# Kernel optimization log

Measured on AMD Instinct MI355X. Metric: run time of the kernel, lower is better.

## Reference

```python
import jax, jax.numpy as jnp
import numpy as np

IN_FEATURES = 16384
OUT_FEATURES = 16384
NNZ = 1_000_000
BATCH = 256


def setup_inputs() -> dict:
    key = jax.random.key(0)
    k1, k2, k3 = jax.random.split(key, 3)
    x = jax.random.normal(k1, (IN_FEATURES, BATCH), dtype=jnp.float32)
    values = jax.random.normal(k2, (NNZ,), dtype=jnp.float32)
    indices = jax.random.randint(k3, (2, NNZ), 0, OUT_FEATURES, dtype=jnp.int64)
    bias = jnp.zeros((OUT_FEATURES, 1), dtype=jnp.float32)
    return {"x": x, "values": values, "indices": indices, "bias": bias}


def reference(x, values, indices, bias):
    # Sparse (COO) matmul: out[r, :] += values[k] * x[c, :] for each nnz (r, c).
    # Equivalent to torch.sparse.mm(W_coo.coalesce(), x) + bias since
    # coalesce() sums duplicate entries and segment_sum does the same.
    row = indices[0]  # [nnz] in [0, OUT_FEATURES)
    col = indices[1]  # [nnz] in [0, IN_FEATURES)
    gathered = values[:, None] * x[col]  # [nnz, B]
    out = jax.ops.segment_sum(gathered, row, num_segments=OUT_FEATURES)  # [out, B]
    return out + bias
```

## Files before the change

### kernel.cpp

```cpp
#include <hip/hip_runtime.h>

typedef unsigned int u32;
typedef unsigned short u16;

constexpr int OUT_F = 16384;
constexpr int IN_F  = 16384;
constexpr int B_N   = 256;
constexpr int NGRP  = 256;
constexpr int GCAP  = 4608;
constexpr int BINB  = 4096;


__global__ __launch_bounds__(1024) void prep_k(
    const int* __restrict__ rows, const int* __restrict__ cols,
    const float* __restrict__ vals, const float* __restrict__ x,
    u16* __restrict__ xb, int* __restrict__ gcnt,
    uint2* __restrict__ gbuck, int nnz, int nbin, int n4) {
  const int tid = threadIdx.x;

  if ((int)blockIdx.x >= nbin) {
    const int i2 = blockIdx.x - nbin;
    for (int j = 0; j < 4; ++j) {
      int k4 = i2 * 4096 + j * 1024 + tid;
      if (k4 < n4) {
        float4 v = ((const float4*)x)[k4];
        u32 u0 = __float_as_uint(v.x), u1 = __float_as_uint(v.y),
            u2 = __float_as_uint(v.z), u3 = __float_as_uint(v.w);
        ushort4 r;
        r.x = (u16)((u0 + 0x7FFFu + ((u0 >> 16) & 1u)) >> 16);
        r.y = (u16)((u1 + 0x7FFFu + ((u1 >> 16) & 1u)) >> 16);
        r.z = (u16)((u2 + 0x7FFFu + ((u2 >> 16) & 1u)) >> 16);
        r.w = (u16)((u3 + 0x7FFFu + ((u3 >> 16) & 1u)) >> 16);
        ((ushort4*)xb)[k4] = r;
      }
    }
    return;
  }

  __shared__ int   hist[NGRP], lofs[NGRP], cur[NGRP], gbase[NGRP], scanb[NGRP];
  __shared__ uint2 stage[BINB];
  __shared__ int   tgt[BINB];

  const int base = blockIdx.x * BINB;
  const int nval = min(BINB, nnz - base);
  if (tid < NGRP) hist[tid] = 0;
  __syncthreads();

  int r[4]; u32 c[4]; float v[4]; bool ok[4];
#pragma unroll
  for (int i = 0; i < 4; ++i) {
    int k = base + i * 1024 + tid;
    ok[i] = k < nnz;
    if (ok[i]) {
      r[i] = rows[k]; c[i] = (u32)cols[k]; v[i] = vals[k];
      atomicAdd(&hist[r[i] >> 6], 1);
    }
  }
  __syncthreads();

  if (tid < NGRP) scanb[tid] = hist[tid];
  __syncthreads();
  for (int off = 1; off < NGRP; off <<= 1) {
    int t = 0;
    if (tid < NGRP && tid >= off) t = scanb[tid - off];
    __syncthreads();
    if (tid < NGRP) scanb[tid] += t;
    __syncthreads();
  }
  if (tid < NGRP) {
    int lo = scanb[tid] - hist[tid];
    lofs[tid] = lo;
    cur[tid]  = lo;
    gbase[tid] = atomicAdd(&gcnt[tid], hist[tid]);
  }
  __syncthreads();

#pragma unroll
  for (int i = 0; i < 4; ++i) {
    if (ok[i]) {
      int g   = r[i] >> 6;
      int pos = atomicAdd(&cur[g], 1);
      stage[pos].x = (c[i] << 6) | (u32)(r[i] & 63);
      stage[pos].y = __float_as_uint(v[i]);
      int w = gbase[g] + (pos - lofs[g]);
      tgt[pos] = (w < GCAP) ? (g * GCAP + w) : -1;
    }
  }
  __syncthreads();

#pragma unroll
  for (int j = 0; j < 4; ++j) {
    int idx = j * 1024 + tid;
    if (idx < nval) {
      int t = tgt[idx];
      if (t >= 0) gbuck[t] = stage[idx];
    }
  }
}

__global__ __launch_bounds__(1024) void regroup_k(
    int* __restrict__ gcnt, uint2* __restrict__ gbuck,
    int* __restrict__ rowstart, int* __restrict__ rowcnt) {
  __shared__ int hist[64], rofs[64], cur[64];
  const int tid = threadIdx.x;
  const int g   = blockIdx.x;
  int cnt = gcnt[g];
  if (cnt > GCAP) cnt = GCAP;
  uint2* bk = gbuck + (size_t)g * GCAP;

  if (tid < 64) hist[tid] = 0;
  __syncthreads();

  uint2 e[5]; bool ok[5];
#pragma unroll
  for (int i = 0; i < 5; ++i) {
    int k = i * 1024 + tid;
    ok[i] = k < cnt;
    if (ok[i]) {
      e[i] = bk[k];
      atomicAdd(&hist[e[i].x & 63u], 1);
    }
  }
  __syncthreads();

  if (tid == 0) {
    int run = 0;
    for (int b = 0; b < 64; ++b) { rofs[b] = run; cur[b] = run; run += hist[b]; }
  }
  __syncthreads();

  if (tid < 64) {
    rowstart[g * 64 + tid] = g * GCAP + rofs[tid];
    rowcnt[g * 64 + tid]   = hist[tid];
  }

#pragma unroll
  for (int i = 0; i < 5; ++i) {
    if (ok[i]) {
      int fr  = (int)(e[i].x & 63u);
      int pos = atomicAdd(&cur[fr], 1);
      bk[pos] = e[i];
    }
  }
}

__global__ __launch_bounds__(256) void spmm_final_k(
    const int* __restrict__ rowstart, const int* __restrict__ rowcnt,
    const uint2* __restrict__ gbuck, const u16* __restrict__ xb,
    const float* __restrict__ bias, float* __restrict__ out) {
  const int lane = threadIdx.x & 63;
  const int wid  = threadIdx.x >> 6;
  const int r    = blockIdx.x * 4 + wid;
  const int cnt  = rowcnt[r];
  const uint2* bk = gbuck + rowstart[r];
  float a0 = 0.f, a1 = 0.f, a2 = 0.f, a3 = 0.f;
  for (int base = 0; base < cnt; base += 64) {
    const int m = min(64, cnt - base);
    uint2 pk = make_uint2(0u, 0u);
    if (lane < m) pk = bk[base + lane];
    int j = 0;
    for (; j + 4 <= m; j += 4) {
      u32 k0 = (u32)__builtin_amdgcn_readlane((int)pk.x, j);
      u32 v0b = (u32)__builtin_amdgcn_readlane((int)pk.y, j);
      u32 k1 = (u32)__builtin_amdgcn_readlane((int)pk.x, j + 1);
      u32 v1b = (u32)__builtin_amdgcn_readlane((int)pk.y, j + 1);
      u32 k2 = (u32)__builtin_amdgcn_readlane((int)pk.x, j + 2);
      u32 v2b = (u32)__builtin_amdgcn_readlane((int)pk.y, j + 2);
      u32 k3 = (u32)__builtin_amdgcn_readlane((int)pk.x, j + 3);
      u32 v3b = (u32)__builtin_amdgcn_readlane((int)pk.y, j + 3);
      uint2 x0 = ((const uint2*)(xb + ((size_t)(k0 >> 6) << 8)))[lane];
      uint2 x1 = ((const uint2*)(xb + ((size_t)(k1 >> 6) << 8)))[lane];
      uint2 x2 = ((const uint2*)(xb + ((size_t)(k2 >> 6) << 8)))[lane];
      uint2 x3 = ((const uint2*)(xb + ((size_t)(k3 >> 6) << 8)))[lane];
      float v0 = __uint_as_float(v0b), v1 = __uint_as_float(v1b);
      float v2 = __uint_as_float(v2b), v3 = __uint_as_float(v3b);
      a0 = fmaf(v0, __uint_as_float(x0.x << 16), a0);
      a1 = fmaf(v0, __uint_as_float(x0.x & 0xFFFF0000u), a1);
      a2 = fmaf(v0, __uint_as_float(x0.y << 16), a2);
      a3 = fmaf(v0, __uint_as_float(x0.y & 0xFFFF0000u), a3);
      a0 = fmaf(v1, __uint_as_float(x1.x << 16), a0);
      a1 = fmaf(v1, __uint_as_float(x1.x & 0xFFFF0000u), a1);
      a2 = fmaf(v1, __uint_as_float(x1.y << 16), a2);
      a3 = fmaf(v1, __uint_as_float(x1.y & 0xFFFF0000u), a3);
      a0 = fmaf(v2, __uint_as_float(x2.x << 16), a0);
      a1 = fmaf(v2, __uint_as_float(x2.x & 0xFFFF0000u), a1);
      a2 = fmaf(v2, __uint_as_float(x2.y << 16), a2);
      a3 = fmaf(v2, __uint_as_float(x2.y & 0xFFFF0000u), a3);
      a0 = fmaf(v3, __uint_as_float(x3.x << 16), a0);
      a1 = fmaf(v3, __uint_as_float(x3.x & 0xFFFF0000u), a1);
      a2 = fmaf(v3, __uint_as_float(x3.y << 16), a2);
      a3 = fmaf(v3, __uint_as_float(x3.y & 0xFFFF0000u), a3);
    }
    for (; j < m; ++j) {
      u32 kk = (u32)__builtin_amdgcn_readlane((int)pk.x, j);
      u32 vb = (u32)__builtin_amdgcn_readlane((int)pk.y, j);
      float v = __uint_as_float(vb);
      uint2 xx = ((const uint2*)(xb + ((size_t)(kk >> 6) << 8)))[lane];
      a0 = fmaf(v, __uint_as_float(xx.x << 16), a0);
      a1 = fmaf(v, __uint_as_float(xx.x & 0xFFFF0000u), a1);
      a2 = fmaf(v, __uint_as_float(xx.y << 16), a2);
      a3 = fmaf(v, __uint_as_float(xx.y & 0xFFFF0000u), a3);
    }
  }
  const float bv = bias[r];
  float4 o;
  o.x = a0 + bv; o.y = a1 + bv; o.z = a2 + bv; o.w = a3 + bv;
  ((float4*)(out + (size_t)r * B_N))[lane] = o;
}


__global__ __launch_bounds__(256) void hist_k(const int* __restrict__ rows,
                                              int* __restrict__ counts, int nnz) {
  int k = blockIdx.x * 256 + threadIdx.x;
  if (k < nnz) atomicAdd(&counts[rows[k]], 1);
}

__global__ __launch_bounds__(1024) void scan_k(const int* __restrict__ counts,
                                               int* __restrict__ offsets,
                                               int* __restrict__ cursor) {
  __shared__ int part[1024];
  const int tid  = threadIdx.x;
  const int base = tid * 16;
  int loc[16];
  int s = 0;
#pragma unroll
  for (int i = 0; i < 16; ++i) { loc[i] = counts[base + i]; s += loc[i]; }
  part[tid] = s;
  __syncthreads();
  for (int off = 1; off < 1024; off <<= 1) {
    int v = (tid >= off) ? part[tid - off] : 0;
    __syncthreads();
    part[tid] += v;
    __syncthreads();
  }
  int run = (tid == 0) ? 0 : part[tid - 1];
#pragma unroll
  for (int i = 0; i < 16; ++i) {
    offsets[base + i] = run;
    cursor[base + i]  = run;
    run += loc[i];
  }
  if (tid == 1023) offsets[OUT_F] = run;
}

__global__ __launch_bounds__(256) void scatter_k(const int* __restrict__ rows,
                                                 const int* __restrict__ colsIn,
                                                 const float* __restrict__ vals,
                                                 int* __restrict__ cursor,
                                                 int* __restrict__ colsOut,
                                                 float* __restrict__ valsOut,
                                                 int nnz) {
  int k = blockIdx.x * 256 + threadIdx.x;
  if (k < nnz) {
    int r   = rows[k];
    int pos = atomicAdd(&cursor[r], 1);
    colsOut[pos] = colsIn[k];
    valsOut[pos] = vals[k];
  }
}

__global__ __launch_bounds__(256) void spmm_k(const int* __restrict__ offsets,
                                              const int* __restrict__ cols,
                                              const float* __restrict__ vals,
                                              const float* __restrict__ x,
                                              const float* __restrict__ bias,
                                              float* __restrict__ out) {
  __shared__ int   c_lds[256];
  __shared__ float v_lds[256];
  const int r = blockIdx.x;
  const int b = threadIdx.x;
  const int start = offsets[r];
  const int end   = offsets[r + 1];
  float acc = 0.f;
  for (int basei = start; basei < end; basei += 256) {
    const int n = min(256, end - basei);
    if (threadIdx.x < n) {
      c_lds[threadIdx.x] = cols[basei + threadIdx.x];
      v_lds[threadIdx.x] = vals[basei + threadIdx.x];
    }
    __syncthreads();
    for (int j = 0; j < n; ++j) {
      acc = fmaf(v_lds[j], x[(size_t)c_lds[j] * B_N + b], acc);
    }
    __syncthreads();
  }
  out[(size_t)r * B_N + b] = acc + bias[r];
}


__global__ __launch_bounds__(256) void initout_k(const float* __restrict__ bias,
                                                 float* __restrict__ out) {
  int i = blockIdx.x * 256 + threadIdx.x;
  out[i] = bias[i >> 8];
}

__global__ __launch_bounds__(256) void atomic_k(const int* __restrict__ rows,
                                                const int* __restrict__ colsIn,
                                                const float* __restrict__ vals,
                                                const float* __restrict__ x,
                                                float* __restrict__ out, int nnz) {
  int k = blockIdx.x;
  if (k < nnz) {
    int r = rows[k], c = colsIn[k];
    float v = vals[k];
    int b = threadIdx.x;
    atomicAdd(&out[(size_t)r * B_N + b], v * x[(size_t)c * B_N + b]);
  }
}

extern "C" void kernel_launch(void* const* d_in, const int* in_sizes, int n_in,
                              void* d_out, int out_size, void* d_ws, size_t ws_size,
                              hipStream_t stream) {
  const float* x      = (const float*)d_in[0];
  const float* values = (const float*)d_in[1];
  const int*   idx    = (const int*)d_in[2];
  const float* bias   = (const float*)d_in[3];
  float* out = (float*)d_out;

  const int nnz = in_sizes[2] / 2;
  const int* rows   = idx;
  const int* colsIn = idx + nnz;

  char* ws = (char*)d_ws;
  auto align256 = [](size_t v) { return (v + 255) & ~(size_t)255; };

  size_t t1_gcnt  = 0;
  size_t t1_rs    = align256(t1_gcnt + (size_t)NGRP * 4);
  size_t t1_rc    = align256(t1_rs + (size_t)OUT_F * 4);
  size_t t1_gbuck = align256(t1_rc + (size_t)OUT_F * 4);
  size_t t1_xb    = align256(t1_gbuck + (size_t)NGRP * GCAP * 8);
  size_t t1_need  = align256(t1_xb + (size_t)IN_F * B_N * 2);

  size_t t2_counts  = 0;
  size_t t2_offsets = align256(t2_counts + (size_t)OUT_F * 4);
  size_t t2_cursor  = align256(t2_offsets + ((size_t)OUT_F + 1) * 4);
  size_t t2_cols    = align256(t2_cursor + (size_t)OUT_F * 4);
  size_t t2_vals    = align256(t2_cols + (size_t)nnz * 4);
  size_t t2_need    = align256(t2_vals + (size_t)nnz * 4);

  if (ws_size >= t1_need) {
    int*   gcnt     = (int*)(ws + t1_gcnt);
    int*   rowstart = (int*)(ws + t1_rs);
    int*   rowcnt   = (int*)(ws + t1_rc);
    uint2* gbuck    = (uint2*)(ws + t1_gbuck);
    u16*   xb       = (u16*)(ws + t1_xb);

    const int n4   = IN_F * B_N / 4;
    const int nbin = (nnz + BINB - 1) / BINB;
    const int nxc  = (n4 + 4095) / 4096;

    hipMemsetAsync(gcnt, 0, (size_t)NGRP * 4, stream);
    prep_k<<<nbin + nxc, 1024, 0, stream>>>(rows, colsIn, values, x, xb, gcnt,
                                            gbuck, nnz, nbin, n4);
    regroup_k<<<NGRP, 1024, 0, stream>>>(gcnt, gbuck, rowstart, rowcnt);
    spmm_final_k<<<OUT_F / 4, 256, 0, stream>>>(rowstart, rowcnt, gbuck, xb,
                                                bias, out);
  } else if (ws_size >= t2_need) {
    int*   counts  = (int*)(ws + t2_counts);
    int*   offsets = (int*)(ws + t2_offsets);
    int*   cursor  = (int*)(ws + t2_cursor);
    int*   colsB   = (int*)(ws + t2_cols);
    float* valsB   = (float*)(ws + t2_vals);

    const int nblk = (nnz + 255) / 256;
    hipMemsetAsync(counts, 0, (size_t)OUT_F * 4, stream);
    hist_k<<<nblk, 256, 0, stream>>>(rows, counts, nnz);
    scan_k<<<1, 1024, 0, stream>>>(counts, offsets, cursor);
    scatter_k<<<nblk, 256, 0, stream>>>(rows, colsIn, values, cursor, colsB, valsB, nnz);
    spmm_k<<<OUT_F, 256, 0, stream>>>(offsets, colsB, valsB, x, bias, out);
  } else {
    initout_k<<<(out_size + 255) / 256, 256, 0, stream>>>(bias, out);
    atomic_k<<<nnz, 256, 0, stream>>>(rows, colsIn, values, x, out, nnz);
  }
}
```

Baseline: 78.30 us.

## Split SpMM over batch halves in two launches with nontemporal bucket loads and stores

The SpMM kernel now runs twice, each launch covering half of the 256 batch columns. Each lane loads one u32 (two bf16 values) per nonzero instead of a uint2, so the working set of x in cache per launch is halved (4 MB bf16 becomes 2 MB per half). Bucket entries are read and outputs written with nontemporal hints so they do not evict x from cache. In exchange, the bucket indices and values are read twice, and there is an extra launch with half the work per lane, which leaves less memory-level parallelism per wave.

```diff
diff --git a/kernel.cpp b/kernel.cpp
--- a/kernel.cpp
+++ b/kernel.cpp
@@ -2,6 +2,7 @@
 
 typedef unsigned int u32;
 typedef unsigned short u16;
+typedef unsigned long long u64;
 
 constexpr int OUT_F = 16384;
 constexpr int IN_F  = 16384;
@@ -144,7 +145,8 @@
   }
 }
 
-__global__ __launch_bounds__(256) void spmm_final_k(
+template <int HALF>
+__global__ __launch_bounds__(256) void spmm_half_k(
     const int* __restrict__ rowstart, const int* __restrict__ rowcnt,
     const uint2* __restrict__ gbuck, const u16* __restrict__ xb,
     const float* __restrict__ bias, float* __restrict__ out) {
@@ -152,60 +154,53 @@
   const int wid  = threadIdx.x >> 6;
   const int r    = blockIdx.x * 4 + wid;
   const int cnt  = rowcnt[r];
-  const uint2* bk = gbuck + rowstart[r];
-  float a0 = 0.f, a1 = 0.f, a2 = 0.f, a3 = 0.f;
+  const u64* bk  = (const u64*)(gbuck + rowstart[r]);
+  const u32* xb32 = (const u32*)xb;
+  float a0 = 0.f, a1 = 0.f;
   for (int base = 0; base < cnt; base += 64) {
     const int m = min(64, cnt - base);
-    uint2 pk = make_uint2(0u, 0u);
-    if (lane < m) pk = bk[base + lane];
+    u64 pk = 0;
+    if (lane < m) pk = __builtin_nontemporal_load(&bk[base + lane]);
+    u32 pkx = (u32)pk, pky = (u32)(pk >> 32);
     int j = 0;
     for (; j + 4 <= m; j += 4) {
-      u32 k0 = (u32)__builtin_amdgcn_readlane((int)pk.x, j);
-      u32 v0b = (u32)__builtin_amdgcn_readlane((int)pk.y, j);
-      u32 k1 = (u32)__builtin_amdgcn_readlane((int)pk.x, j + 1);
-      u32 v1b = (u32)__builtin_amdgcn_readlane((int)pk.y, j + 1);
-      u32 k2 = (u32)__builtin_amdgcn_readlane((int)pk.x, j + 2);
-      u32 v2b = (u32)__builtin_amdgcn_readlane((int)pk.y, j + 2);
-      u32 k3 = (u32)__builtin_amdgcn_readlane((int)pk.x, j + 3);
-      u32 v3b = (u32)__builtin_amdgcn_readlane((int)pk.y, j + 3);
-      uint2 x0 = ((const uint2*)(xb + ((size_t)(k0 >> 6) << 8)))[lane];
-      uint2 x1 = ((const uint2*)(xb + ((size_t)(k1 >> 6) << 8)))[lane];
-      uint2 x2 = ((const uint2*)(xb + ((size_t)(k2 >> 6) << 8)))[lane];
-      uint2 x3 = ((const uint2*)(xb + ((size_t)(k3 >> 6) << 8)))[lane];
+      u32 k0  = (u32)__builtin_amdgcn_readlane((int)pkx, j);
+      u32 v0b = (u32)__builtin_amdgcn_readlane((int)pky, j);
+      u32 k1  = (u32)__builtin_amdgcn_readlane((int)pkx, j + 1);
+      u32 v1b = (u32)__builtin_amdgcn_readlane((int)pky, j + 1);
+      u32 k2  = (u32)__builtin_amdgcn_readlane((int)pkx, j + 2);
+      u32 v2b = (u32)__builtin_amdgcn_readlane((int)pky, j + 2);
+      u32 k3  = (u32)__builtin_amdgcn_readlane((int)pkx, j + 3);
+      u32 v3b = (u32)__builtin_amdgcn_readlane((int)pky, j + 3);
+      u32 x0 = xb32[((size_t)(k0 >> 6) << 7) | (HALF << 6) | lane];
+      u32 x1 = xb32[((size_t)(k1 >> 6) << 7) | (HALF << 6) | lane];
+      u32 x2 = xb32[((size_t)(k2 >> 6) << 7) | (HALF << 6) | lane];
+      u32 x3 = xb32[((size_t)(k3 >> 6) << 7) | (HALF << 6) | lane];
       float v0 = __uint_as_float(v0b), v1 = __uint_as_float(v1b);
       float v2 = __uint_as_float(v2b), v3 = __uint_as_float(v3b);
-      a0 = fmaf(v0, __uint_as_float(x0.x << 16), a0);
-      a1 = fmaf(v0, __uint_as_float(x0.x & 0xFFFF0000u), a1);
-      a2 = fmaf(v0, __uint_as_float(x0.y << 16), a2);
-      a3 = fmaf(v0, __uint_as_float(x0.y & 0xFFFF0000u), a3);
-      a0 = fmaf(v1, __uint_as_float(x1.x << 16), a0);
-      a1 = fmaf(v1, __uint_as_float(x1.x & 0xFFFF0000u), a1);
-      a2 = fmaf(v1, __uint_as_float(x1.y << 16), a2);
-      a3 = fmaf(v1, __uint_as_float(x1.y & 0xFFFF0000u), a3);
-      a0 = fmaf(v2, __uint_as_float(x2.x << 16), a0);
-      a1 = fmaf(v2, __uint_as_float(x2.x & 0xFFFF0000u), a1);
-      a2 = fmaf(v2, __uint_as_float(x2.y << 16), a2);
-      a3 = fmaf(v2, __uint_as_float(x2.y & 0xFFFF0000u), a3);
-      a0 = fmaf(v3, __uint_as_float(x3.x << 16), a0);
-      a1 = fmaf(v3, __uint_as_float(x3.x & 0xFFFF0000u), a1);
-      a2 = fmaf(v3, __uint_as_float(x3.y << 16), a2);
-      a3 = fmaf(v3, __uint_as_float(x3.y & 0xFFFF0000u), a3);
+      a0 = fmaf(v0, __uint_as_float(x0 << 16), a0);
+      a1 = fmaf(v0, __uint_as_float(x0 & 0xFFFF0000u), a1);
+      a0 = fmaf(v1, __uint_as_float(x1 << 16), a0);
+      a1 = fmaf(v1, __uint_as_float(x1 & 0xFFFF0000u), a1);
+      a0 = fmaf(v2, __uint_as_float(x2 << 16), a0);
+      a1 = fmaf(v2, __uint_as_float(x2 & 0xFFFF0000u), a1);
+      a0 = fmaf(v3, __uint_as_float(x3 << 16), a0);
+      a1 = fmaf(v3, __uint_as_float(x3 & 0xFFFF0000u), a1);
     }
     for (; j < m; ++j) {
-      u32 kk = (u32)__builtin_amdgcn_readlane((int)pk.x, j);
-      u32 vb = (u32)__builtin_amdgcn_readlane((int)pk.y, j);
+      u32 kk = (u32)__builtin_amdgcn_readlane((int)pkx, j);
+      u32 vb = (u32)__builtin_amdgcn_readlane((int)pky, j);
       float v = __uint_as_float(vb);
-      uint2 xx = ((const uint2*)(xb + ((size_t)(kk >> 6) << 8)))[lane];
-      a0 = fmaf(v, __uint_as_float(xx.x << 16), a0);
-      a1 = fmaf(v, __uint_as_float(xx.x & 0xFFFF0000u), a1);
-      a2 = fmaf(v, __uint_as_float(xx.y << 16), a2);
-      a3 = fmaf(v, __uint_as_float(xx.y & 0xFFFF0000u), a3);
+      u32 xx = xb32[((size_t)(kk >> 6) << 7) | (HALF << 6) | lane];
+      a0 = fmaf(v, __uint_as_float(xx << 16), a0);
+      a1 = fmaf(v, __uint_as_float(xx & 0xFFFF0000u), a1);
     }
   }
   const float bv = bias[r];
-  float4 o;
-  o.x = a0 + bv; o.y = a1 + bv; o.z = a2 + bv; o.w = a3 + bv;
-  ((float4*)(out + (size_t)r * B_N))[lane] = o;
+  float o0 = a0 + bv, o1 = a1 + bv;
+  u64 packed = ((u64)__float_as_uint(o1) << 32) | (u64)__float_as_uint(o0);
+  u64* dst = (u64*)(out + (size_t)r * B_N + HALF * 128 + lane * 2);
+  __builtin_nontemporal_store(packed, dst);
 }
 
 
@@ -353,8 +348,10 @@
     prep_k<<<nbin + nxc, 1024, 0, stream>>>(rows, colsIn, values, x, xb, gcnt,
                                             gbuck, nnz, nbin, n4);
     regroup_k<<<NGRP, 1024, 0, stream>>>(gcnt, gbuck, rowstart, rowcnt);
-    spmm_final_k<<<OUT_F / 4, 256, 0, stream>>>(rowstart, rowcnt, gbuck, xb,
-                                                bias, out);
+    spmm_half_k<0><<<OUT_F / 4, 256, 0, stream>>>(rowstart, rowcnt, gbuck, xb,
+                                                  bias, out);
+    spmm_half_k<1><<<OUT_F / 4, 256, 0, stream>>>(rowstart, rowcnt, gbuck, xb,
+                                                  bias, out);
   } else if (ws_size >= t2_need) {
     int*   counts  = (int*)(ws + t2_counts);
     int*   offsets = (int*)(ws + t2_offsets);
```

After: 87.26 us. 1.11x slower.
